# Kernel tuning notes

Hardware: AMD Instinct MI355X
Metric: run time of the kernel (lower is better)

The kernel has to match this reference:

```python
import jax, jax.numpy as jnp
import numpy as np

N_NODES = 100000


def _lightgcn_layer(x, src, dst, norm):
    # message: norm * x[src]; aggregate: mean over incoming edges at dst
    msg = norm[:, None] * x[src]                                   # [E+N, D]
    s = jax.ops.segment_sum(msg, dst, num_segments=N_NODES)        # [N, D]
    cnt = jax.ops.segment_sum(jnp.ones_like(norm), dst, num_segments=N_NODES)
    return s / cnt[:, None]                                        # deg>=1 due to self-loops


def _graph_embeddings(emb, edge_index):
    n = emb.shape[0]
    loop = jnp.arange(n, dtype=edge_index.dtype)
    src = jnp.concatenate([edge_index[0], loop])                   # self-loops appended
    dst = jnp.concatenate([edge_index[1], loop])
    deg = jax.ops.segment_sum(jnp.ones(src.shape[0], emb.dtype), src, num_segments=N_NODES)
    dis = deg ** -0.5
    norm = dis[src] * dis[dst]
    x = emb
    acc = emb
    for _ in range(2):  # num_layers
        x = _lightgcn_layer(x, src, dst, norm)
        acc = acc + x
    return acc / 3.0  # mean over (num_layers + 1) embeddings


def setup_inputs() -> dict:
    key = jax.random.key(0)
    k1, k2, k3, k4 = jax.random.split(key, 4)
    emb = jax.random.normal(k1, (N_NODES, 128), dtype=jnp.float32) * 0.02
    edge_index = jax.random.randint(k2, (2, 600000), 0, N_NODES, dtype=jnp.int64)
    items = jax.random.randint(k3, (4096, 1), 0, N_NODES, dtype=jnp.int64)
    samples = jax.random.randint(k4, (4096, 100), 0, N_NODES, dtype=jnp.int64)
    return {"emb": emb, "edge_index": edge_index, "items": items, "samples": samples}


def reference(emb, edge_index, items, samples):
    embeddings = _graph_embeddings(emb, edge_index)                # [N, D]
    item_emb = embeddings[items]                                   # [B, 1, D]
    sample_emb = embeddings[samples]                               # [B, S, D]
    scores = jnp.einsum('bod,bsd->bos', item_emb, sample_emb)      # [B, 1, S]
    return scores.squeeze(1)                                       # [B, S]
```

## Files before the change

kernel.cpp:

```cpp
#include <hip/hip_runtime.h>

#define NN 100000
#define D 128
#define W 32

__device__ __forceinline__ unsigned short f2bf(float f) {
    unsigned u = __float_as_uint(f);
    u += 0x7FFF + ((u >> 16) & 1);
    return (unsigned short)(u >> 16);
}
__device__ __forceinline__ float bf2f(unsigned short h) {
    return __uint_as_float(((unsigned)h) << 16);
}
__device__ __forceinline__ unsigned pack2(float a, float b) {
    return (unsigned)f2bf(a) | ((unsigned)f2bf(b) << 16);
}

__global__ __launch_bounds__(256) void hetero_kernel(const int* __restrict__ src,
                                                     const int* __restrict__ dst,
                                                     const float* __restrict__ emb,
                                                     int* __restrict__ deg,
                                                     int* __restrict__ fillc,
                                                     int* __restrict__ ell,
                                                     unsigned short* __restrict__ y0h,
                                                     int E, int EB, int total8) {
    int b = blockIdx.x;
    if (b < EB) {
        int e = b * 256 + threadIdx.x;
        if (e < E) {
            int s = src[e], d = dst[e];
            atomicAdd(&deg[s], 1);
            int pos = atomicAdd(&fillc[d], 1);
            if (pos < W) ell[(size_t)d * W + pos] = s;
        }
    } else {
        int t = (b - EB) * 256 + threadIdx.x;
        if (t < total8) {
            const float4 a = ((const float4*)emb)[t * 2];
            const float4 c = ((const float4*)emb)[t * 2 + 1];
            uint4 o;
            o.x = pack2(a.x, a.y);
            o.y = pack2(a.z, a.w);
            o.z = pack2(c.x, c.y);
            o.w = pack2(c.z, c.w);
            ((uint4*)y0h)[t] = o;
        }
    }
}

__global__ __launch_bounds__(256) void gather1_kernel(const int* __restrict__ ell,
                                                      const int* __restrict__ fillc,
                                                      const int* __restrict__ deg,
                                                      const unsigned short* __restrict__ y0h,
                                                      unsigned short* __restrict__ y1h, int n) {
    unsigned t = blockIdx.x * 256u + threadIdx.x;
    unsigned i = t >> 5, q = t & 31u;
    if (i >= (unsigned)n) return;
    int len = fillc[i];
    int lenc = len > W ? W : len;
    const int* base = ell + (size_t)i * W;
    float wd = rsqrtf((float)deg[i] + 1.0f);
    const ushort4 ph = *(const ushort4*)(y0h + (size_t)i * D + q * 4);
    float4 acc = {wd * bf2f(ph.x), wd * bf2f(ph.y), wd * bf2f(ph.z), wd * bf2f(ph.w)};
    int j = 0;
    for (; j + 4 <= lenc; j += 4) {
        const int4 ss = *(const int4*)(base + j);
        float w0 = rsqrtf((float)deg[ss.x] + 1.0f);
        float w1 = rsqrtf((float)deg[ss.y] + 1.0f);
        float w2 = rsqrtf((float)deg[ss.z] + 1.0f);
        float w3 = rsqrtf((float)deg[ss.w] + 1.0f);
        const ushort4 v0 = *(const ushort4*)(y0h + (size_t)ss.x * D + q * 4);
        const ushort4 v1 = *(const ushort4*)(y0h + (size_t)ss.y * D + q * 4);
        const ushort4 v2 = *(const ushort4*)(y0h + (size_t)ss.z * D + q * 4);
        const ushort4 v3 = *(const ushort4*)(y0h + (size_t)ss.w * D + q * 4);
        acc.x += w0 * bf2f(v0.x) + w1 * bf2f(v1.x) + w2 * bf2f(v2.x) + w3 * bf2f(v3.x);
        acc.y += w0 * bf2f(v0.y) + w1 * bf2f(v1.y) + w2 * bf2f(v2.y) + w3 * bf2f(v3.y);
        acc.z += w0 * bf2f(v0.z) + w1 * bf2f(v1.z) + w2 * bf2f(v2.z) + w3 * bf2f(v3.z);
        acc.w += w0 * bf2f(v0.w) + w1 * bf2f(v1.w) + w2 * bf2f(v2.w) + w3 * bf2f(v3.w);
    }
    for (; j < lenc; ++j) {
        int s0 = base[j];
        float w0 = rsqrtf((float)deg[s0] + 1.0f);
        const ushort4 v0 = *(const ushort4*)(y0h + (size_t)s0 * D + q * 4);
        acc.x += w0 * bf2f(v0.x);
        acc.y += w0 * bf2f(v0.y);
        acc.z += w0 * bf2f(v0.z);
        acc.w += w0 * bf2f(v0.w);
    }
    float ci = 1.0f / (float)(len + 1);
    float f1 = ci * wd * wd;
    ushort4 o;
    o.x = f2bf(f1 * acc.x);
    o.y = f2bf(f1 * acc.y);
    o.z = f2bf(f1 * acc.z);
    o.w = f2bf(f1 * acc.w);
    *(ushort4*)(y1h + (size_t)i * D + q * 4) = o;
}

__global__ __launch_bounds__(256) void gather2_kernel(const int* __restrict__ ell,
                                                      const int* __restrict__ fillc,
                                                      const int* __restrict__ deg,
                                                      const unsigned short* __restrict__ y1h,
                                                      const float* __restrict__ emb,
                                                      unsigned short* __restrict__ finh, int n) {
    unsigned t = blockIdx.x * 256u + threadIdx.x;
    unsigned i = t >> 5, q = t & 31u;
    if (i >= (unsigned)n) return;
    int len = fillc[i];
    int lenc = len > W ? W : len;
    const int* base = ell + (size_t)i * W;
    const ushort4 ph = *(const ushort4*)(y1h + (size_t)i * D + q * 4);
    float sx = bf2f(ph.x), sy = bf2f(ph.y), sz = bf2f(ph.z), sw = bf2f(ph.w);
    float4 acc = {sx, sy, sz, sw};
    int j = 0;
    for (; j + 4 <= lenc; j += 4) {
        const int4 ss = *(const int4*)(base + j);
        const ushort4 v0 = *(const ushort4*)(y1h + (size_t)ss.x * D + q * 4);
        const ushort4 v1 = *(const ushort4*)(y1h + (size_t)ss.y * D + q * 4);
        const ushort4 v2 = *(const ushort4*)(y1h + (size_t)ss.z * D + q * 4);
        const ushort4 v3 = *(const ushort4*)(y1h + (size_t)ss.w * D + q * 4);
        acc.x += (bf2f(v0.x) + bf2f(v1.x)) + (bf2f(v2.x) + bf2f(v3.x));
        acc.y += (bf2f(v0.y) + bf2f(v1.y)) + (bf2f(v2.y) + bf2f(v3.y));
        acc.z += (bf2f(v0.z) + bf2f(v1.z)) + (bf2f(v2.z) + bf2f(v3.z));
        acc.w += (bf2f(v0.w) + bf2f(v1.w)) + (bf2f(v2.w) + bf2f(v3.w));
    }
    for (; j < lenc; ++j) {
        int s0 = base[j];
        const ushort4 v0 = *(const ushort4*)(y1h + (size_t)s0 * D + q * 4);
        acc.x += bf2f(v0.x);
        acc.y += bf2f(v0.y);
        acc.z += bf2f(v0.z);
        acc.w += bf2f(v0.w);
    }
    float dp1 = (float)deg[i] + 1.0f;
    float wd = rsqrtf(dp1);
    float wdi = sqrtf(dp1);
    float ci = 1.0f / (float)(len + 1);
    float g = ci * wd;
    const float4 e = *(const float4*)(emb + (size_t)i * D + q * 4);
    const float k = 1.0f / 3.0f;
    ushort4 o;
    o.x = f2bf((e.x + sx * wdi + g * acc.x) * k);
    o.y = f2bf((e.y + sy * wdi + g * acc.y) * k);
    o.z = f2bf((e.z + sz * wdi + g * acc.z) * k);
    o.w = f2bf((e.w + sw * wdi + g * acc.w) * k);
    *(ushort4*)(finh + (size_t)i * D + q * 4) = o;
}

__global__ __launch_bounds__(256) void scores_kernel(const unsigned short* __restrict__ finh,
                                                     const int* __restrict__ items,
                                                     const int* __restrict__ samples,
                                                     float* __restrict__ out, int S) {
    __shared__ float it[D];
    int b = blockIdx.x;
    if (threadIdx.x < D) it[threadIdx.x] = bf2f(finh[(size_t)items[b] * D + threadIdx.x]);
    __syncthreads();
    int hw = threadIdx.x >> 5, lane = threadIdx.x & 31;
    const float4 w = *(const float4*)(it + lane * 4);
    int s = hw;
    for (; s + 8 < S; s += 16) {
        int node0 = samples[b * S + s];
        int node1 = samples[b * S + s + 8];
        const ushort4 v0 = *(const ushort4*)(finh + (size_t)node0 * D + lane * 4);
        const ushort4 v1 = *(const ushort4*)(finh + (size_t)node1 * D + lane * 4);
        float a0 = bf2f(v0.x) * w.x + bf2f(v0.y) * w.y + bf2f(v0.z) * w.z + bf2f(v0.w) * w.w;
        float a1 = bf2f(v1.x) * w.x + bf2f(v1.y) * w.y + bf2f(v1.z) * w.z + bf2f(v1.w) * w.w;
        #pragma unroll
        for (int o = 16; o; o >>= 1) {
            a0 += __shfl_xor(a0, o);
            a1 += __shfl_xor(a1, o);
        }
        if (lane == 0) {
            out[b * S + s] = a0;
            out[b * S + s + 8] = a1;
        }
    }
    if (s < S) {
        int node = samples[b * S + s];
        const ushort4 v = *(const ushort4*)(finh + (size_t)node * D + lane * 4);
        float acc = bf2f(v.x) * w.x + bf2f(v.y) * w.y + bf2f(v.z) * w.z + bf2f(v.w) * w.w;
        #pragma unroll
        for (int o = 16; o; o >>= 1) acc += __shfl_xor(acc, o);
        if (lane == 0) out[b * S + s] = acc;
    }
}

extern "C" void kernel_launch(void* const* d_in, const int* in_sizes, int n_in,
                              void* d_out, int out_size, void* d_ws, size_t ws_size,
                              hipStream_t stream) {
    const float* emb = (const float*)d_in[0];
    const int* ei = (const int*)d_in[1];
    const int* items = (const int*)d_in[2];
    const int* samples = (const int*)d_in[3];
    float* out = (float*)d_out;

    const int E = in_sizes[1] / 2;
    const int B = in_sizes[2];
    const int S = in_sizes[3] / B;
    const int* src = ei;
    const int* dst = ei + E;

    int* deg = (int*)d_ws;
    int* fillc = deg + NN;
    int* ell = fillc + NN;
    unsigned short* y0h = (unsigned short*)(ell + (size_t)NN * W);
    unsigned short* y1h = y0h + (size_t)NN * D;
    unsigned short* finh = y1h + (size_t)NN * D;

    hipMemsetAsync(deg, 0, 2 * NN * sizeof(int), stream);

    const int EB = (E + 255) / 256;
    const int total8 = NN * D / 8;
    const int CB = (total8 + 255) / 256;
    hetero_kernel<<<EB + CB, 256, 0, stream>>>(src, dst, emb, deg, fillc, ell, y0h, E, EB, total8);

    const int gblocks = (NN * 32 + 255) / 256;
    gather1_kernel<<<gblocks, 256, 0, stream>>>(ell, fillc, deg, y0h, y1h, NN);
    gather2_kernel<<<gblocks, 256, 0, stream>>>(ell, fillc, deg, y1h, emb, finh, NN);

    scores_kernel<<<B, 256, 0, stream>>>(finh, items, samples, out, S);
}
```

Before: 172.6 us.

## Build degree and ELL adjacency via two-level binned counting sort

Replaces per-edge global atomics for degree counting and ELL slot filling with a bucketed counting sort. Edges are histogrammed into 128-node coarse bins in shared memory, prefix-scanned, scattered into binned arrays, then a per-bin kernel uses shared-memory atomics to compute degrees and fill ELL rows. This removes contended global atomics and the memset, at the cost of three extra kernel launches, a serial single-block scan, and extra scratch traffic. Neighbor order within ELL rows changes, which can alter float summation order.

```diff
diff --git a/kernel.cpp b/kernel.cpp
--- a/kernel.cpp
+++ b/kernel.cpp
@@ -3,6 +3,9 @@
 #define NN 100000
 #define D 128
 #define W 32
+#define NB 96
+#define NBIN 1024
+#define FBIN 782
 
 __device__ __forceinline__ unsigned short f2bf(float f) {
     unsigned u = __float_as_uint(f);
@@ -16,25 +19,28 @@
     return (unsigned)f2bf(a) | ((unsigned)f2bf(b) << 16);
 }
 
-__global__ __launch_bounds__(256) void hetero_kernel(const int* __restrict__ src,
-                                                     const int* __restrict__ dst,
-                                                     const float* __restrict__ emb,
-                                                     int* __restrict__ deg,
-                                                     int* __restrict__ fillc,
-                                                     int* __restrict__ ell,
-                                                     unsigned short* __restrict__ y0h,
-                                                     int E, int EB, int total8) {
+__global__ __launch_bounds__(256) void hist_kernel(const int* __restrict__ src,
+                                                   const int* __restrict__ dst,
+                                                   const float* __restrict__ emb,
+                                                   int* __restrict__ bh,
+                                                   unsigned short* __restrict__ y0h,
+                                                   int E, int chunk, int total8) {
     int b = blockIdx.x;
-    if (b < EB) {
-        int e = b * 256 + threadIdx.x;
-        if (e < E) {
-            int s = src[e], d = dst[e];
-            atomicAdd(&deg[s], 1);
-            int pos = atomicAdd(&fillc[d], 1);
-            if (pos < W) ell[(size_t)d * W + pos] = s;
+    if (b < NB) {
+        __shared__ int hA[NBIN], hB[NBIN];
+        for (int t = threadIdx.x; t < NBIN; t += 256) { hA[t] = 0; hB[t] = 0; }
+        __syncthreads();
+        int s0 = b * chunk, s1 = min(s0 + chunk, E);
+        for (int e = s0 + (int)threadIdx.x; e < s1; e += 256) {
+            atomicAdd(&hA[src[e] >> 7], 1);
+            atomicAdd(&hB[dst[e] >> 7], 1);
         }
+        __syncthreads();
+        int* gA = bh + (size_t)b * NBIN;
+        int* gB = bh + (size_t)(NB + b) * NBIN;
+        for (int t = threadIdx.x; t < NBIN; t += 256) { gA[t] = hA[t]; gB[t] = hB[t]; }
     } else {
-        int t = (b - EB) * 256 + threadIdx.x;
+        int t = (b - NB) * 256 + threadIdx.x;
         if (t < total8) {
             const float4 a = ((const float4*)emb)[t * 2];
             const float4 c = ((const float4*)emb)[t * 2 + 1];
@@ -45,6 +51,81 @@
             o.w = pack2(c.z, c.w);
             ((uint4*)y0h)[t] = o;
         }
+    }
+}
+
+__global__ __launch_bounds__(1024) void scan_kernel(int* __restrict__ bh,
+                                                    int* __restrict__ binstart, int E) {
+    __shared__ int ws[16];
+    int t = threadIdx.x, lane = t & 63, w = t >> 6;
+    for (int ks = 0; ks < 2; ++ks) {
+        int* h = bh + (size_t)ks * NB * NBIN;
+        int sum = 0;
+        for (int b = 0; b < NB; ++b) sum += h[b * NBIN + t];
+        int v = sum;
+        #pragma unroll
+        for (int o = 1; o < 64; o <<= 1) { int y = __shfl_up(v, o); if (lane >= o) v += y; }
+        if (lane == 63) ws[w] = v;
+        __syncthreads();
+        int add = 0;
+        for (int k = 0; k < w; ++k) add += ws[k];
+        int incl = v + add;
+        int base = incl - sum;
+        binstart[ks * 1025 + t] = base;
+        if (t == 1023) binstart[ks * 1025 + 1024] = incl;
+        int run = base;
+        for (int b = 0; b < NB; ++b) { int x = h[b * NBIN + t]; h[b * NBIN + t] = run; run += x; }
+        __syncthreads();
+    }
+}
+
+__global__ __launch_bounds__(256) void scatter_kernel(const int* __restrict__ src,
+                                                      const int* __restrict__ dst,
+                                                      const int* __restrict__ bh,
+                                                      unsigned char* __restrict__ sfine,
+                                                      unsigned int* __restrict__ packed,
+                                                      int E, int chunk) {
+    __shared__ int offA[NBIN], offB[NBIN];
+    int b = blockIdx.x;
+    const int* gA = bh + (size_t)b * NBIN;
+    const int* gB = bh + (size_t)(NB + b) * NBIN;
+    for (int t = threadIdx.x; t < NBIN; t += 256) { offA[t] = gA[t]; offB[t] = gB[t]; }
+    __syncthreads();
+    int s0 = b * chunk, s1 = min(s0 + chunk, E);
+    for (int e = s0 + (int)threadIdx.x; e < s1; e += 256) {
+        int s = src[e], d = dst[e];
+        int pa = atomicAdd(&offA[s >> 7], 1);
+        sfine[pa] = (unsigned char)(s & 127);
+        int pb = atomicAdd(&offB[d >> 7], 1);
+        packed[pb] = (unsigned)s | ((unsigned)(d & 127) << 17);
+    }
+}
+
+__global__ __launch_bounds__(256) void fine_kernel(const unsigned char* __restrict__ sfine,
+                                                   const unsigned int* __restrict__ packed,
+                                                   const int* __restrict__ binstart,
+                                                   int* __restrict__ deg,
+                                                   int* __restrict__ fillc,
+                                                   int* __restrict__ ell, int n) {
+    __shared__ int hist[128], cnt[128];
+    int b = blockIdx.x;
+    if (threadIdx.x < 128) { hist[threadIdx.x] = 0; cnt[threadIdx.x] = 0; }
+    __syncthreads();
+    int a0 = binstart[b], a1 = binstart[b + 1];
+    for (int p = a0 + (int)threadIdx.x; p < a1; p += 256)
+        atomicAdd(&hist[sfine[p]], 1);
+    int b0 = binstart[1025 + b], b1 = binstart[1025 + b + 1];
+    for (int p = b0 + (int)threadIdx.x; p < b1; p += 256) {
+        unsigned v = packed[p];
+        int f = (v >> 17) & 127;
+        int s = (int)(v & 0x1FFFF);
+        int slot = atomicAdd(&cnt[f], 1);
+        if (slot < W) ell[(size_t)(b * 128 + f) * W + slot] = s;
+    }
+    __syncthreads();
+    if (threadIdx.x < 128) {
+        int node = b * 128 + threadIdx.x;
+        if (node < n) { deg[node] = hist[threadIdx.x]; fillc[node] = cnt[threadIdx.x]; }
     }
 }
 
@@ -200,19 +281,25 @@
     const int* src = ei;
     const int* dst = ei + E;
 
-    int* deg = (int*)d_ws;
+    int* bh = (int*)d_ws;
+    int* binstart = bh + 2 * NB * NBIN;
+    int* deg = binstart + 2052;
     int* fillc = deg + NN;
     int* ell = fillc + NN;
-    unsigned short* y0h = (unsigned short*)(ell + (size_t)NN * W);
+    unsigned char* sfine = (unsigned char*)(ell + (size_t)NN * W);
+    unsigned int* packed = (unsigned int*)(sfine + ((E + 3) & ~3));
+    unsigned short* y0h = (unsigned short*)(packed + E);
     unsigned short* y1h = y0h + (size_t)NN * D;
     unsigned short* finh = y1h + (size_t)NN * D;
 
-    hipMemsetAsync(deg, 0, 2 * NN * sizeof(int), stream);
-
-    const int EB = (E + 255) / 256;
+    const int chunk = (E + NB - 1) / NB;
     const int total8 = NN * D / 8;
     const int CB = (total8 + 255) / 256;
-    hetero_kernel<<<EB + CB, 256, 0, stream>>>(src, dst, emb, deg, fillc, ell, y0h, E, EB, total8);
+
+    hist_kernel<<<NB + CB, 256, 0, stream>>>(src, dst, emb, bh, y0h, E, chunk, total8);
+    scan_kernel<<<1, 1024, 0, stream>>>(bh, binstart, E);
+    scatter_kernel<<<NB, 256, 0, stream>>>(src, dst, bh, sfine, packed, E, chunk);
+    fine_kernel<<<FBIN, 256, 0, stream>>>(sfine, packed, binstart, deg, fillc, ell, NN);
 
     const int gblocks = (NN * 32 + 255) / 256;
     gather1_kernel<<<gblocks, 256, 0, stream>>>(ell, fillc, deg, y0h, y1h, NN);
```

New measurement: 185.1 us. 1.07x slower.

## Widen bf16 row loads to 16 bytes and interleave hetero kernel block roles

Applied to the files above, without the earlier changes.

The gather and scoring kernels now assign 16 lanes per 128-wide row, each loading a uint4 (8 bf16 values) instead of a ushort4. This halves thread count and doubles per-load width, which reduces load instructions and index and weight recomputation per row. The hetero kernel also interleaves edge-processing blocks with conversion blocks across the grid instead of placing them contiguously, so atomic-heavy blocks and streaming blocks run concurrently. The costs are fewer threads available for hiding gather latency and more registers per thread.

```diff
diff --git a/kernel.cpp b/kernel.cpp
--- a/kernel.cpp
+++ b/kernel.cpp
@@ -9,11 +9,16 @@
     u += 0x7FFF + ((u >> 16) & 1);
     return (unsigned short)(u >> 16);
 }
-__device__ __forceinline__ float bf2f(unsigned short h) {
-    return __uint_as_float(((unsigned)h) << 16);
-}
+__device__ __forceinline__ float bflo(unsigned u) { return __uint_as_float(u << 16); }
+__device__ __forceinline__ float bfhi(unsigned u) { return __uint_as_float(u & 0xFFFF0000u); }
 __device__ __forceinline__ unsigned pack2(float a, float b) {
     return (unsigned)f2bf(a) | ((unsigned)f2bf(b) << 16);
+}
+__device__ __forceinline__ void addrow(float* acc, const uint4 v, float w) {
+    acc[0] += w * bflo(v.x); acc[1] += w * bfhi(v.x);
+    acc[2] += w * bflo(v.y); acc[3] += w * bfhi(v.y);
+    acc[4] += w * bflo(v.z); acc[5] += w * bfhi(v.z);
+    acc[6] += w * bflo(v.w); acc[7] += w * bfhi(v.w);
 }
 
 __global__ __launch_bounds__(256) void hetero_kernel(const int* __restrict__ src,
@@ -23,10 +28,12 @@
                                                      int* __restrict__ fillc,
                                                      int* __restrict__ ell,
                                                      unsigned short* __restrict__ y0h,
-                                                     int E, int EB, int total8) {
+                                                     int E, int EB, int total, int total8) {
     int b = blockIdx.x;
-    if (b < EB) {
-        int e = b * 256 + threadIdx.x;
+    int lo = (int)(((long long)b * EB) / total);
+    int hi = (int)(((long long)(b + 1) * EB) / total);
+    if (hi > lo) {
+        int e = lo * 256 + threadIdx.x;
         if (e < E) {
             int s = src[e], d = dst[e];
             atomicAdd(&deg[s], 1);
@@ -34,7 +41,7 @@
             if (pos < W) ell[(size_t)d * W + pos] = s;
         }
     } else {
-        int t = (b - EB) * 256 + threadIdx.x;
+        int t = (b - hi) * 256 + threadIdx.x;
         if (t < total8) {
             const float4 a = ((const float4*)emb)[t * 2];
             const float4 c = ((const float4*)emb)[t * 2 + 1];
@@ -54,14 +61,15 @@
                                                       const unsigned short* __restrict__ y0h,
                                                       unsigned short* __restrict__ y1h, int n) {
     unsigned t = blockIdx.x * 256u + threadIdx.x;
-    unsigned i = t >> 5, q = t & 31u;
+    unsigned i = t >> 4, q = t & 15u;
     if (i >= (unsigned)n) return;
     int len = fillc[i];
     int lenc = len > W ? W : len;
     const int* base = ell + (size_t)i * W;
     float wd = rsqrtf((float)deg[i] + 1.0f);
-    const ushort4 ph = *(const ushort4*)(y0h + (size_t)i * D + q * 4);
-    float4 acc = {wd * bf2f(ph.x), wd * bf2f(ph.y), wd * bf2f(ph.z), wd * bf2f(ph.w)};
+    const uint4 ph = *(const uint4*)(y0h + (size_t)i * D + q * 8);
+    float acc[8] = {0.f, 0.f, 0.f, 0.f, 0.f, 0.f, 0.f, 0.f};
+    addrow(acc, ph, wd);
     int j = 0;
     for (; j + 4 <= lenc; j += 4) {
         const int4 ss = *(const int4*)(base + j);
@@ -69,32 +77,29 @@
         float w1 = rsqrtf((float)deg[ss.y] + 1.0f);
         float w2 = rsqrtf((float)deg[ss.z] + 1.0f);
         float w3 = rsqrtf((float)deg[ss.w] + 1.0f);
-        const ushort4 v0 = *(const ushort4*)(y0h + (size_t)ss.x * D + q * 4);
-        const ushort4 v1 = *(const ushort4*)(y0h + (size_t)ss.y * D + q * 4);
-        const ushort4 v2 = *(const ushort4*)(y0h + (size_t)ss.z * D + q * 4);
-        const ushort4 v3 = *(const ushort4*)(y0h + (size_t)ss.w * D + q * 4);
-        acc.x += w0 * bf2f(v0.x) + w1 * bf2f(v1.x) + w2 * bf2f(v2.x) + w3 * bf2f(v3.x);
-        acc.y += w0 * bf2f(v0.y) + w1 * bf2f(v1.y) + w2 * bf2f(v2.y) + w3 * bf2f(v3.y);
-        acc.z += w0 * bf2f(v0.z) + w1 * bf2f(v1.z) + w2 * bf2f(v2.z) + w3 * bf2f(v3.z);
-        acc.w += w0 * bf2f(v0.w) + w1 * bf2f(v1.w) + w2 * bf2f(v2.w) + w3 * bf2f(v3.w);
+        const uint4 v0 = *(const uint4*)(y0h + (size_t)ss.x * D + q * 8);
+        const uint4 v1 = *(const uint4*)(y0h + (size_t)ss.y * D + q * 8);
+        const uint4 v2 = *(const uint4*)(y0h + (size_t)ss.z * D + q * 8);
+        const uint4 v3 = *(const uint4*)(y0h + (size_t)ss.w * D + q * 8);
+        addrow(acc, v0, w0);
+        addrow(acc, v1, w1);
+        addrow(acc, v2, w2);
+        addrow(acc, v3, w3);
     }
     for (; j < lenc; ++j) {
         int s0 = base[j];
         float w0 = rsqrtf((float)deg[s0] + 1.0f);
-        const ushort4 v0 = *(const ushort4*)(y0h + (size_t)s0 * D + q * 4);
-        acc.x += w0 * bf2f(v0.x);
-        acc.y += w0 * bf2f(v0.y);
-        acc.z += w0 * bf2f(v0.z);
-        acc.w += w0 * bf2f(v0.w);
+        const uint4 v0 = *(const uint4*)(y0h + (size_t)s0 * D + q * 8);
+        addrow(acc, v0, w0);
     }
     float ci = 1.0f / (float)(len + 1);
     float f1 = ci * wd * wd;
-    ushort4 o;
-    o.x = f2bf(f1 * acc.x);
-    o.y = f2bf(f1 * acc.y);
-    o.z = f2bf(f1 * acc.z);
-    o.w = f2bf(f1 * acc.w);
-    *(ushort4*)(y1h + (size_t)i * D + q * 4) = o;
+    uint4 o;
+    o.x = pack2(f1 * acc[0], f1 * acc[1]);
+    o.y = pack2(f1 * acc[2], f1 * acc[3]);
+    o.z = pack2(f1 * acc[4], f1 * acc[5]);
+    o.w = pack2(f1 * acc[6], f1 * acc[7]);
+    *(uint4*)(y1h + (size_t)i * D + q * 8) = o;
 }
 
 __global__ __launch_bounds__(256) void gather2_kernel(const int* __restrict__ ell,
@@ -104,47 +109,60 @@
                                                       const float* __restrict__ emb,
                                                       unsigned short* __restrict__ finh, int n) {
     unsigned t = blockIdx.x * 256u + threadIdx.x;
-    unsigned i = t >> 5, q = t & 31u;
+    unsigned i = t >> 4, q = t & 15u;
     if (i >= (unsigned)n) return;
     int len = fillc[i];
     int lenc = len > W ? W : len;
     const int* base = ell + (size_t)i * W;
-    const ushort4 ph = *(const ushort4*)(y1h + (size_t)i * D + q * 4);
-    float sx = bf2f(ph.x), sy = bf2f(ph.y), sz = bf2f(ph.z), sw = bf2f(ph.w);
-    float4 acc = {sx, sy, sz, sw};
+    const uint4 ph = *(const uint4*)(y1h + (size_t)i * D + q * 8);
+    float self[8];
+    self[0] = bflo(ph.x); self[1] = bfhi(ph.x);
+    self[2] = bflo(ph.y); self[3] = bfhi(ph.y);
+    self[4] = bflo(ph.z); self[5] = bfhi(ph.z);
+    self[6] = bflo(ph.w); self[7] = bfhi(ph.w);
+    float acc[8];
+    #pragma unroll
+    for (int k = 0; k < 8; ++k) acc[k] = self[k];
     int j = 0;
     for (; j + 4 <= lenc; j += 4) {
         const int4 ss = *(const int4*)(base + j);
-        const ushort4 v0 = *(const ushort4*)(y1h + (size_t)ss.x * D + q * 4);
-        const ushort4 v1 = *(const ushort4*)(y1h + (size_t)ss.y * D + q * 4);
-        const ushort4 v2 = *(const ushort4*)(y1h + (size_t)ss.z * D + q * 4);
-        const ushort4 v3 = *(const ushort4*)(y1h + (size_t)ss.w * D + q * 4);
-        acc.x += (bf2f(v0.x) + bf2f(v1.x)) + (bf2f(v2.x) + bf2f(v3.x));
-        acc.y += (bf2f(v0.y) + bf2f(v1.y)) + (bf2f(v2.y) + bf2f(v3.y));
-        acc.z += (bf2f(v0.z) + bf2f(v1.z)) + (bf2f(v2.z) + bf2f(v3.z));
-        acc.w += (bf2f(v0.w) + bf2f(v1.w)) + (bf2f(v2.w) + bf2f(v3.w));
+        const uint4 v0 = *(const uint4*)(y1h + (size_t)ss.x * D + q * 8);
+        const uint4 v1 = *(const uint4*)(y1h + (size_t)ss.y * D + q * 8);
+        const uint4 v2 = *(const uint4*)(y1h + (size_t)ss.z * D + q * 8);
+        const uint4 v3 = *(const uint4*)(y1h + (size_t)ss.w * D + q * 8);
+        addrow(acc, v0, 1.0f);
+        addrow(acc, v1, 1.0f);
+        addrow(acc, v2, 1.0f);
+        addrow(acc, v3, 1.0f);
     }
     for (; j < lenc; ++j) {
         int s0 = base[j];
-        const ushort4 v0 = *(const ushort4*)(y1h + (size_t)s0 * D + q * 4);
-        acc.x += bf2f(v0.x);
-        acc.y += bf2f(v0.y);
-        acc.z += bf2f(v0.z);
-        acc.w += bf2f(v0.w);
+        const uint4 v0 = *(const uint4*)(y1h + (size_t)s0 * D + q * 8);
+        addrow(acc, v0, 1.0f);
     }
     float dp1 = (float)deg[i] + 1.0f;
     float wd = rsqrtf(dp1);
     float wdi = sqrtf(dp1);
     float ci = 1.0f / (float)(len + 1);
     float g = ci * wd;
-    const float4 e = *(const float4*)(emb + (size_t)i * D + q * 4);
-    const float k = 1.0f / 3.0f;
-    ushort4 o;
-    o.x = f2bf((e.x + sx * wdi + g * acc.x) * k);
-    o.y = f2bf((e.y + sy * wdi + g * acc.y) * k);
-    o.z = f2bf((e.z + sz * wdi + g * acc.z) * k);
-    o.w = f2bf((e.w + sw * wdi + g * acc.w) * k);
-    *(ushort4*)(finh + (size_t)i * D + q * 4) = o;
+    const float4 e0 = *(const float4*)(emb + (size_t)i * D + q * 8);
+    const float4 e1 = *(const float4*)(emb + (size_t)i * D + q * 8 + 4);
+    const float k3 = 1.0f / 3.0f;
+    float r[8];
+    r[0] = (e0.x + self[0] * wdi + g * acc[0]) * k3;
+    r[1] = (e0.y + self[1] * wdi + g * acc[1]) * k3;
+    r[2] = (e0.z + self[2] * wdi + g * acc[2]) * k3;
+    r[3] = (e0.w + self[3] * wdi + g * acc[3]) * k3;
+    r[4] = (e1.x + self[4] * wdi + g * acc[4]) * k3;
+    r[5] = (e1.y + self[5] * wdi + g * acc[5]) * k3;
+    r[6] = (e1.z + self[6] * wdi + g * acc[6]) * k3;
+    r[7] = (e1.w + self[7] * wdi + g * acc[7]) * k3;
+    uint4 o;
+    o.x = pack2(r[0], r[1]);
+    o.y = pack2(r[2], r[3]);
+    o.z = pack2(r[4], r[5]);
+    o.w = pack2(r[6], r[7]);
+    *(uint4*)(finh + (size_t)i * D + q * 8) = o;
 }
 
 __global__ __launch_bounds__(256) void scores_kernel(const unsigned short* __restrict__ finh,
@@ -153,35 +171,44 @@
                                                      float* __restrict__ out, int S) {
     __shared__ float it[D];
     int b = blockIdx.x;
-    if (threadIdx.x < D) it[threadIdx.x] = bf2f(finh[(size_t)items[b] * D + threadIdx.x]);
+    if (threadIdx.x < 64) {
+        unsigned u = ((const unsigned*)(finh + (size_t)items[b] * D))[threadIdx.x];
+        it[threadIdx.x * 2] = bflo(u);
+        it[threadIdx.x * 2 + 1] = bfhi(u);
+    }
     __syncthreads();
-    int hw = threadIdx.x >> 5, lane = threadIdx.x & 31;
-    const float4 w = *(const float4*)(it + lane * 4);
-    int s = hw;
-    for (; s + 8 < S; s += 16) {
+    int g = threadIdx.x >> 4, lane = threadIdx.x & 15;
+    float w[8];
+    #pragma unroll
+    for (int k = 0; k < 8; ++k) w[k] = it[lane * 8 + k];
+    int s = g;
+    for (; s + 16 < S; s += 32) {
         int node0 = samples[b * S + s];
-        int node1 = samples[b * S + s + 8];
-        const ushort4 v0 = *(const ushort4*)(finh + (size_t)node0 * D + lane * 4);
-        const ushort4 v1 = *(const ushort4*)(finh + (size_t)node1 * D + lane * 4);
-        float a0 = bf2f(v0.x) * w.x + bf2f(v0.y) * w.y + bf2f(v0.z) * w.z + bf2f(v0.w) * w.w;
-        float a1 = bf2f(v1.x) * w.x + bf2f(v1.y) * w.y + bf2f(v1.z) * w.z + bf2f(v1.w) * w.w;
+        int node1 = samples[b * S + s + 16];
+        const uint4 v0 = *(const uint4*)(finh + (size_t)node0 * D + lane * 8);
+        const uint4 v1 = *(const uint4*)(finh + (size_t)node1 * D + lane * 8);
+        float a0 = w[0] * bflo(v0.x) + w[1] * bfhi(v0.x) + w[2] * bflo(v0.y) + w[3] * bfhi(v0.y)
+                 + w[4] * bflo(v0.z) + w[5] * bfhi(v0.z) + w[6] * bflo(v0.w) + w[7] * bfhi(v0.w);
+        float a1 = w[0] * bflo(v1.x) + w[1] * bfhi(v1.x) + w[2] * bflo(v1.y) + w[3] * bfhi(v1.y)
+                 + w[4] * bflo(v1.z) + w[5] * bfhi(v1.z) + w[6] * bflo(v1.w) + w[7] * bfhi(v1.w);
         #pragma unroll
-        for (int o = 16; o; o >>= 1) {
+        for (int o = 8; o; o >>= 1) {
             a0 += __shfl_xor(a0, o);
             a1 += __shfl_xor(a1, o);
         }
         if (lane == 0) {
             out[b * S + s] = a0;
-            out[b * S + s + 8] = a1;
+            out[b * S + s + 16] = a1;
         }
     }
     if (s < S) {
         int node = samples[b * S + s];
-        const ushort4 v = *(const ushort4*)(finh + (size_t)node * D + lane * 4);
-        float acc = bf2f(v.x) * w.x + bf2f(v.y) * w.y + bf2f(v.z) * w.z + bf2f(v.w) * w.w;
+        const uint4 v = *(const uint4*)(finh + (size_t)node * D + lane * 8);
+        float a = w[0] * bflo(v.x) + w[1] * bfhi(v.x) + w[2] * bflo(v.y) + w[3] * bfhi(v.y)
+                + w[4] * bflo(v.z) + w[5] * bfhi(v.z) + w[6] * bflo(v.w) + w[7] * bfhi(v.w);
         #pragma unroll
-        for (int o = 16; o; o >>= 1) acc += __shfl_xor(acc, o);
-        if (lane == 0) out[b * S + s] = acc;
+        for (int o = 8; o; o >>= 1) a += __shfl_xor(a, o);
+        if (lane == 0) out[b * S + s] = a;
     }
 }
 
@@ -212,9 +239,11 @@
     const int EB = (E + 255) / 256;
     const int total8 = NN * D / 8;
     const int CB = (total8 + 255) / 256;
-    hetero_kernel<<<EB + CB, 256, 0, stream>>>(src, dst, emb, deg, fillc, ell, y0h, E, EB, total8);
-
-    const int gblocks = (NN * 32 + 255) / 256;
+    const int total = EB + CB;
+    hetero_kernel<<<total, 256, 0, stream>>>(src, dst, emb, deg, fillc, ell, y0h,
+                                             E, EB, total, total8);
+
+    const int gblocks = (NN * 16 + 255) / 256;
     gather1_kernel<<<gblocks, 256, 0, stream>>>(ell, fillc, deg, y0h, y1h, NN);
     gather2_kernel<<<gblocks, 256, 0, stream>>>(ell, fillc, deg, y1h, emb, finh, NN);
 
```

Measured after the change: 152.9 us. -11.4%, faster.
